# Kernel optimization log

Measured on AMD Instinct MI355X. Metric: run time of the kernel, lower is better.

Reference implementation:

```python
import jax, jax.numpy as jnp
import numpy as np

B, N, IN_CH = 4, 8192, 4
K = 16
W0, W1, W2 = 64, 128, 256
NUM_CLASSES = 3


def setup_inputs() -> dict:
    key = jax.random.key(0)
    ks = jax.random.split(key, 16)

    def lin(kw, kb, fan_in, fan_out):
        bound = 1.0 / np.sqrt(fan_in)
        w = jax.random.uniform(kw, (fan_in, fan_out), jnp.float32, -bound, bound)
        b = jax.random.uniform(kb, (fan_out,), jnp.float32, -bound, bound)
        return w, b

    x = jax.random.normal(ks[0], (B, N, IN_CH), jnp.float32)
    stem_w, stem_b = lin(ks[1], ks[2], IN_CH, W0)
    b1_w, b1_b = lin(ks[3], ks[4], 2 * W0 + 3, W1)
    b2_w, b2_b = lin(ks[5], ks[6], 2 * W1 + 3, W2)
    glob_w, glob_b = lin(ks[7], ks[8], W2, W2)
    head1_w, head1_b = lin(ks[9], ks[10], 2 * W2, W2)
    head2_w, head2_b = lin(ks[11], ks[12], W2, NUM_CLASSES)
    return {
        'x': x,
        'hmix_a': jnp.float32(1.0), 'hmix_b': jnp.float32(1.0), 'hmix_c': jnp.float32(0.0),
        'stem_w': stem_w, 'stem_b': stem_b,
        'b1_w': b1_w, 'b1_b': b1_b,
        'b2_w': b2_w, 'b2_b': b2_b,
        'glob_w': glob_w, 'glob_b': glob_b,
        'head1_w': head1_w, 'head1_b': head1_b,
        'head2_w': head2_w, 'head2_b': head2_b,
        'thresh': jnp.float32(0.15), 'sharp': jnp.float32(10.0), 'scale': jnp.float32(0.5),
    }


def _knn_idx(coords, k):
    # coords: [B,N,3] -> idx of k nearest neighbors (incl. self), no grad.
    c = jax.lax.stop_gradient(coords)
    xx = jnp.sum(c * c, axis=-1, keepdims=True)            # [B,N,1]
    dist = xx + jnp.swapaxes(xx, 1, 2) - 2.0 * jnp.einsum('bnc,bmc->bnm', c, c)
    dist = jnp.maximum(dist, 0.0)
    _, idx = jax.lax.top_k(-dist, k)                       # smallest distances
    return idx                                             # [B,N,k]


def _local_agg(coords, feat, idx, w, b):
    # gather-concat-MLP-maxpool, faithful to LocalAggBlock (pool='max')
    bidx = jnp.arange(coords.shape[0])[:, None, None]
    nb_f = feat[bidx, idx]                                 # [B,N,k,C]
    nb_p = coords[bidx, idx]                               # [B,N,k,3]
    fi = feat[:, :, None, :]
    pi = coords[:, :, None, :]
    h = jnp.concatenate(
        [jnp.broadcast_to(fi, nb_f.shape), nb_f - fi, nb_p - pi], axis=-1)
    h = jax.nn.relu(jnp.einsum('bnkd,do->bnko', h, w) + b)
    return jnp.max(h, axis=2)                              # [B,N,out]


def reference(x, hmix_a, hmix_b, hmix_c, stem_w, stem_b, b1_w, b1_b,
              b2_w, b2_b, glob_w, glob_b, head1_w, head1_b,
              head2_w, head2_b, thresh, sharp, scale):
    # HeightMixer: z_eff = a*z + b*hag + c
    z_eff = hmix_a * x[..., 2] + hmix_b * x[..., 3] + hmix_c
    coords = jnp.stack([x[..., 0], x[..., 1], z_eff], axis=-1)  # [B,N,3]

    f = jax.nn.relu(x @ stem_w + stem_b)                   # stem: [B,N,64]

    # both blocks use the same coords -> same KNN graph; compute once
    idx = _knn_idx(coords, K)
    f = _local_agg(coords, f, idx, b1_w, b1_b)             # [B,N,128]
    f = _local_agg(coords, f, idx, b2_w, b2_b)             # [B,N,256]

    g = jnp.max(f, axis=1)                                 # [B,256]
    g = jax.nn.relu(g @ glob_w + glob_b)
    g = jnp.broadcast_to(g[:, None, :], f.shape)           # [B,N,256]

    h = jnp.concatenate([f, g], axis=-1)                   # [B,N,512]
    h = jax.nn.relu(h @ head1_w + head1_b)
    logits = h @ head2_w + head2_b                         # [B,N,3]

    # HeightPriorBias on class 0
    hag = x[..., 3]
    bias = scale * jax.nn.sigmoid(sharp * (thresh - hag))
    logits = logits.at[..., 0].add(bias)
    return logits
```

## Files before the change

kernel.cpp:

```cpp
#include <hip/hip_runtime.h>
#include <math.h>

typedef unsigned long long u64;
typedef unsigned int u32;
typedef _Float16 h8v __attribute__((ext_vector_type(8)));
typedef float    f4v __attribute__((ext_vector_type(4)));
typedef float    f16v __attribute__((ext_vector_type(16)));
typedef float    f2v __attribute__((ext_vector_type(2)));

#define MFMA16(a,b,c) __builtin_amdgcn_mfma_f32_16x16x32_f16(a, b, c, 0, 0, 0)
#define MFMA32(a,b,c) __builtin_amdgcn_mfma_f32_32x32x16_f16(a, b, c, 0, 0, 0)

#define B_ 4
#define N_ 8192
#define K_ 16
#define W0_ 64
#define W1_ 128
#define W2_ 256
#define X0_ 96
#define X1_ 160
#define QAD_ 16
#define CAP_ 128

__global__ __launch_bounds__(256) void prep_kernel(
    const float* __restrict__ x,
    const float* __restrict__ stem_w, const float* __restrict__ stem_b,
    const float* __restrict__ hmix_a, const float* __restrict__ hmix_b,
    const float* __restrict__ hmix_c,
    float* __restrict__ coords4, _Float16* __restrict__ fx0,
    _Float16* __restrict__ fx1,
    const float* __restrict__ b1_w, const float* __restrict__ b2_w,
    const float* __restrict__ h1w,
    _Float16* __restrict__ w1m, _Float16* __restrict__ w1d,
    _Float16* __restrict__ w2m, _Float16* __restrict__ w2d,
    _Float16* __restrict__ h1wT,
    _Float16* __restrict__ qa, _Float16* __restrict__ cbq,
    float* __restrict__ part) {
  const int bi = blockIdx.x;
  const int tid = threadIdx.x;
  const int PB = (B_*N_)/4;
  if (bi < PB) {
    const int p = bi * 4 + (tid >> 6);
    const int o = tid & 63;
    const float x0 = x[p*4+0], x1 = x[p*4+1], x2 = x[p*4+2], x3 = x[p*4+3];
    const float z = hmix_a[0]*x2 + hmix_b[0]*x3 + hmix_c[0];
    float acc = stem_b[o] + x0*stem_w[0*W0_+o] + x1*stem_w[1*W0_+o]
              + x2*stem_w[2*W0_+o] + x3*stem_w[3*W0_+o];
    fx0[p*X0_+o] = (_Float16)fmaxf(acc, 0.f);
    if (o < 32) {
      const float tv = (o==0) ? x0 : (o==1) ? x1 : (o==2) ? z : 0.f;
      fx0[p*X0_+W0_+o] = (_Float16)tv;
      fx1[(size_t)p*X1_+W1_+o] = (_Float16)tv;
    }
    if (o == 0) {
      const float xx = x0*x0 + x1*x1 + z*z;
      ((float4*)coords4)[p] = make_float4(x0, x1, z, xx);
    } else if (o == 1) {
      const _Float16 hx = (_Float16)x0, hy = (_Float16)x1, hz = (_Float16)z;
      const _Float16 lx = (_Float16)(x0 - (float)hx);
      const _Float16 ly = (_Float16)(x1 - (float)hy);
      const _Float16 lz = (_Float16)(z  - (float)hz);
      const _Float16 one = (_Float16)1.f, Z = (_Float16)0.f;
      h8v a0 = {hx, hy, hz, lx, ly, lz, hx, hy};
      h8v a1 = {hz, lx, ly, lz, one, one, Z, Z};
      *(h8v*)(qa + (size_t)p*QAD_)      = a0;
      *(h8v*)(qa + (size_t)p*QAD_ + 8)  = a1;
    } else if (o == 2) {
      const _Float16 hx = (_Float16)x0, hy = (_Float16)x1, hz = (_Float16)z;
      const _Float16 lx = (_Float16)(x0 - (float)hx);
      const _Float16 ly = (_Float16)(x1 - (float)hy);
      const _Float16 lz = (_Float16)(z  - (float)hz);
      const float xx = x0*x0 + x1*x1 + z*z;
      const _Float16 xh = (_Float16)xx;
      const _Float16 xl = (_Float16)(xx - (float)xh);
      const _Float16 nhx = (_Float16)(-2.f*(float)hx);
      const _Float16 nhy = (_Float16)(-2.f*(float)hy);
      const _Float16 nhz = (_Float16)(-2.f*(float)hz);
      const _Float16 nlx = (_Float16)(-2.f*(float)lx);
      const _Float16 nly = (_Float16)(-2.f*(float)ly);
      const _Float16 nlz = (_Float16)(-2.f*(float)lz);
      const _Float16 Z = (_Float16)0.f;
      h8v b0 = {nhx, nhy, nhz, nlx, nly, nlz, nlx, nly};
      h8v b1 = {nlz, nhx, nhy, nhz, xh, xl, Z, Z};
      *(h8v*)(cbq + (size_t)p*QAD_)      = b0;
      *(h8v*)(cbq + (size_t)p*QAD_ + 8)  = b1;
    }
  } else if (bi < PB + W1_) {
    const int o = bi - PB, c = tid;
    if (c < X0_) {
      float mv = 0.f, dv = 0.f;
      if (c < W0_)        { const float wm = b1_w[(W0_+c)*W1_+o]; mv = wm; dv = b1_w[c*W1_+o] - wm; }
      else if (c < W0_+3) { const float wp = b1_w[(2*W0_+(c-W0_))*W1_+o]; mv = wp; dv = -wp; }
      w1m[o*X0_+c] = (_Float16)mv;
      w1d[o*X0_+c] = (_Float16)dv;
    }
  } else if (bi < PB + W1_ + W2_) {
    const int o = bi - PB - W1_, c = tid;
    if (c < X1_) {
      float mv = 0.f, dv = 0.f;
      if (c < W1_)        { const float wm = b2_w[(W1_+c)*W2_+o]; mv = wm; dv = b2_w[c*W2_+o] - wm; }
      else if (c < W1_+3) { const float wp = b2_w[(2*W1_+(c-W1_))*W2_+o]; mv = wp; dv = -wp; }
      w2m[o*X1_+c] = (_Float16)mv;
      w2d[o*X1_+c] = (_Float16)dv;
    }
  } else if (bi < PB + W1_ + 2*W2_) {
    const int o = bi - PB - W1_ - W2_;
    for (int c = tid; c < 512; c += 256)
      h1wT[(size_t)o*512 + c] = (_Float16)h1w[(size_t)c*256 + o];
  } else {
    ((float4*)part)[tid] = make_float4(0.f, 0.f, 0.f, 0.f);
  }
}

#define DPP_MIN(v, ctrl)                                                        \
  { const int _t = __builtin_amdgcn_update_dpp(0, __float_as_int(v),            \
      ctrl, 0xF, 0xF, false);                                                   \
    v = fminf(v, __int_as_float(_t)); }

__device__ __forceinline__ float sixteenth_of_minima(float v) {
  float th = 0.f;
#pragma unroll
  for (int r = 0; r < 16; ++r) {
    float w = v;
    DPP_MIN(w, 0x111); DPP_MIN(w, 0x112); DPP_MIN(w, 0x114); DPP_MIN(w, 0x118);
    DPP_MIN(w, 0x142); DPP_MIN(w, 0x143);
    const float mv = __int_as_float(
        __builtin_amdgcn_readlane(__float_as_int(w), 63));
    th = mv;
    v = (v == mv) ? INFINITY : v;
  }
  return th;
}

#define KNN_DIST2(dA, dB)                                                       \
  const f2v cjx = {cj.x, cj.x}, cjy = {cj.y, cj.y},                             \
            cjz = {cj.z, cj.z}, cjw = {cj.w, cj.w};                             \
  f2v tA = cAx * cjx;                                                           \
  tA = __builtin_elementwise_fma(cAy, cjy, tA);                                 \
  tA = __builtin_elementwise_fma(cAz, cjz, tA);                                 \
  const f2v dA = __builtin_elementwise_fma(tA, m2, cAw + cjw);                  \
  f2v tB = cBx * cjx;                                                           \
  tB = __builtin_elementwise_fma(cBy, cjy, tB);                                 \
  tB = __builtin_elementwise_fma(cBz, cjz, tB);                                 \
  const f2v dB = __builtin_elementwise_fma(tB, m2, cBw + cjw);

__global__ __launch_bounds__(512) void knn_kernel(
    const float* __restrict__ coords4, const _Float16* __restrict__ qa,
    const _Float16* __restrict__ cbq, int* __restrict__ knn_idx) {
  const int tid = threadIdx.x;
  const int wid = tid >> 6;
  const int lane = tid & 63;
  const int p0 = blockIdx.x * 32;
  const int bb = (p0 >> 13) << 13;

  __shared__ float  s_Tp[32];
  __shared__ float  s_Tpr[32];
  __shared__ int    s_cnt[32];
  __shared__ float2 s_pr[32][CAP_];
  if (tid < 32) s_cnt[tid] = 0;

  const float4* cb = ((const float4*)coords4) + bb;
  const int q0 = p0 + wid * 4;
  const float4 c0 = ((const float4*)coords4)[q0+0];
  const float4 c1 = ((const float4*)coords4)[q0+1];
  const float4 c2 = ((const float4*)coords4)[q0+2];
  const float4 c3 = ((const float4*)coords4)[q0+3];
  const f2v m2 = {-2.f, -2.f};
  const f2v cAx = {c0.x, c1.x}, cAy = {c0.y, c1.y}, cAz = {c0.z, c1.z}, cAw = {c0.w, c1.w};
  const f2v cBx = {c2.x, c3.x}, cBy = {c2.y, c3.y}, cBz = {c2.z, c3.z}, cBw = {c2.w, c3.w};

  float lm0 = INFINITY, lm1 = INFINITY, lm2 = INFINITY, lm3 = INFINITY;
  for (int it = 0; it < 64; ++it) {
    const float4 cj = cb[it*64 + lane];
    KNN_DIST2(dA, dB)
    lm0 = fminf(lm0, fmaxf(dA[0], 0.f));
    lm1 = fminf(lm1, fmaxf(dA[1], 0.f));
    lm2 = fminf(lm2, fmaxf(dB[0], 0.f));
    lm3 = fminf(lm3, fmaxf(dB[1], 0.f));
  }
  const float Th0 = sixteenth_of_minima(lm0);
  const float Th1 = sixteenth_of_minima(lm1);
  const float Th2 = sixteenth_of_minima(lm2);
  const float Th3 = sixteenth_of_minima(lm3);
  if (lane == 0) {
    s_Tp[wid*4+0] = Th0 - c0.w + (1e-3f + 1e-5f*c0.w);
    s_Tp[wid*4+1] = Th1 - c1.w + (1e-3f + 1e-5f*c1.w);
    s_Tp[wid*4+2] = Th2 - c2.w + (1e-3f + 1e-5f*c2.w);
    s_Tp[wid*4+3] = Th3 - c3.w + (1e-3f + 1e-5f*c3.w);
  }
  __syncthreads();
  if (tid < 32) {
    const int h = tid >> 4, r = tid & 15;
    s_Tpr[tid] = s_Tp[(r&3) + 8*(r>>2) + 4*h];
  }
  __syncthreads();

  const int half = lane >> 5;
  const int h4 = half << 2;
  const int lrow = lane & 31;
  float Tv[16];
  *(f4v*)&Tv[0]  = *(const f4v*)&s_Tpr[half*16 + 0];
  *(f4v*)&Tv[4]  = *(const f4v*)&s_Tpr[half*16 + 4];
  *(f4v*)&Tv[8]  = *(const f4v*)&s_Tpr[half*16 + 8];
  *(f4v*)&Tv[12] = *(const f4v*)&s_Tpr[half*16 + 12];
  const h8v afrag = *(const h8v*)(qa + (size_t)(p0 + lrow)*QAD_ + half*8);
  const int c0b = wid * 1024;
  const int cibase = c0b + lrow;
  const _Float16* cbp = cbq + (size_t)(bb + c0b + lrow)*QAD_ + half*8;
  const f16v zacc = (f16v)0.0f;

  h8v bcur = *(const h8v*)cbp;
#pragma unroll 2
  for (int t = 0; t < 32; ++t) {
    const h8v bnxt = *(const h8v*)(cbp + (size_t)((t < 31) ? (t+1) : 0) * 32 * QAD_);
    const f16v acc = MFMA32(afrag, bcur, zacc);
#pragma unroll
    for (int r = 0; r < 16; ++r) {
      const bool c = acc[r] < Tv[r];
      const u64 m = __ballot(c);
      if (m) {
        const int q = ((r&3) + 8*(r>>2)) + h4;
        if (c) {
          const int pos = atomicAdd(&s_cnt[q], 1);
          if (pos < CAP_)
            s_pr[q][pos] = make_float2(acc[r], __int_as_float(cibase + t*32));
        }
      }
    }
    bcur = bnxt;
  }
  __syncthreads();

  for (int qq = 0; qq < 4; ++qq) {
    const int q = wid*4 + qq;
    const int cnt = s_cnt[q];
    const int L = (cnt < CAP_) ? cnt : CAP_;
    float d0 = INFINITY, d1 = INFINITY;
    int   i0 = 0x7fffffff, i1 = 0x7fffffff;
    if (lane < L)      { const float2 e = s_pr[q][lane];      d0 = e.x; i0 = __float_as_int(e.y); }
    if (lane + 64 < L) { const float2 e = s_pr[q][lane + 64]; d1 = e.x; i1 = __float_as_int(e.y); }
    int keep = 0;
    for (int r = 0; r < K_; ++r) {
      float dl = d0; int il = i0; bool s1 = false;
      if (d1 < dl || (d1 == dl && i1 < il)) { dl = d1; il = i1; s1 = true; }
      float w = dl;
      DPP_MIN(w, 0x111); DPP_MIN(w, 0x112); DPP_MIN(w, 0x114); DPP_MIN(w, 0x118);
      DPP_MIN(w, 0x142); DPP_MIN(w, 0x143);
      const float dmin = __int_as_float(
          __builtin_amdgcn_readlane(__float_as_int(w), 63));
      u64 m = __ballot(dl == dmin);
      int bi = 0x7fffffff, bl = 0;
      do {
        const int s = (int)__ffsll((unsigned long long)m) - 1; m &= m - 1;
        const int ii = __builtin_amdgcn_readlane(il, s);
        if (ii < bi) { bi = ii; bl = s; }
      } while (m);
      if (lane == bl) { if (s1) d1 = INFINITY; else d0 = INFINITY; }
      if (lane == r) keep = bi;
    }
    if (lane < K_) knn_idx[(size_t)(p0 + q)*K_ + lane] = keep;
  }
}

template<int KS, int NPASS, bool GMAX>
__global__ __launch_bounds__(256) void aggm_kernel(
    const _Float16* __restrict__ fx, const int* __restrict__ knn_idx,
    const _Float16* __restrict__ midT, const _Float16* __restrict__ difT,
    const float* __restrict__ bw,
    _Float16* __restrict__ fo, const int ostr, u32* __restrict__ part) {
  const int XD  = KS*32;
  const int XDP = XD + 8;
  const int CH  = KS*4;
  const int p0 = blockIdx.x * 16;
  const int bb = (p0 >> 13) << 13;
  const int tid = threadIdx.x;
  const int w = tid >> 6, lane = tid & 63, col = lane & 15, quad = lane >> 4;
  const int koff = quad * 8;

  __shared__ int s_idx[256];
  __shared__ _Float16 sA[2][64*(KS*32+8)];

  s_idx[tid] = knn_idx[p0*K_ + tid];

  f4v cacc[NPASS][2];
  {
    h8v Ao[KS];
    const _Float16* ap = fx + (size_t)(p0+col)*XD + koff;
#pragma unroll
    for (int kk = 0; kk < KS; ++kk) Ao[kk] = *(const h8v*)(ap + kk*32);
#pragma unroll
    for (int ps = 0; ps < NPASS; ++ps) {
      const int o0 = ps*128 + w*32;
      const _Float16* b0 = difT + (size_t)(o0 + col)*XD + koff;
      const _Float16* b1 = difT + (size_t)(o0 + 16 + col)*XD + koff;
      f4v c0 = {0.f,0.f,0.f,0.f}, c1 = {0.f,0.f,0.f,0.f};
#pragma unroll
      for (int kk = 0; kk < KS; ++kk) {
        c0 = MFMA16(Ao[kk], *(const h8v*)(b0 + kk*32), c0);
        c1 = MFMA16(Ao[kk], *(const h8v*)(b1 + kk*32), c1);
      }
      cacc[ps][0] = c0; cacc[ps][1] = c1;
    }
  }

  h8v Bf[NPASS][2][KS];
  float bias[NPASS][2];
#pragma unroll
  for (int ps = 0; ps < NPASS; ++ps) {
    const int o0 = ps*128 + w*32;
#pragma unroll
    for (int kk = 0; kk < KS; ++kk) {
      Bf[ps][0][kk] = *(const h8v*)(midT + (size_t)(o0 + col)*XD + kk*32 + koff);
      Bf[ps][1][kk] = *(const h8v*)(midT + (size_t)(o0 + 16 + col)*XD + kk*32 + koff);
    }
    bias[ps][0] = bw[o0 + col];
    bias[ps][1] = bw[o0 + 16 + col];
  }
  __syncthreads();

  for (int c = tid; c < 64*CH; c += 256) {
    const int r = c / CH, o = c - r*CH;
    *(uint4*)&sA[0][r*XDP + o*8] =
        *(const uint4*)(fx + (size_t)(bb + s_idx[((r&15)<<4) + (r>>4)])*XD + o*8);
  }
  __syncthreads();

  f4v M[NPASS][2];
#pragma unroll
  for (int ps = 0; ps < NPASS; ++ps) {
    M[ps][0] = (f4v){-INFINITY,-INFINITY,-INFINITY,-INFINITY};
    M[ps][1] = (f4v){-INFINITY,-INFINITY,-INFINITY,-INFINITY};
  }

  for (int s = 0; s < 4; ++s) {
    const int buf = s & 1;
    if (s < 3) {
      for (int c = tid; c < 64*CH; c += 256) {
        const int r = c / CH, o = c - r*CH;
        *(uint4*)&sA[buf^1][r*XDP + o*8] =
            *(const uint4*)(fx + (size_t)(bb + s_idx[((r&15)<<4) + 4*s+4 + (r>>4)])*XD + o*8);
      }
    }
#pragma unroll
    for (int half = 0; half < 4; ++half) {
      h8v Ac[KS];
      const _Float16* ap = &sA[buf][(half*16 + col)*XDP + koff];
#pragma unroll
      for (int kk = 0; kk < KS; ++kk) Ac[kk] = *(const h8v*)(ap + kk*32);
#pragma unroll
      for (int ps = 0; ps < NPASS; ++ps) {
        f4v d0 = {0.f,0.f,0.f,0.f}, d1 = {0.f,0.f,0.f,0.f};
#pragma unroll
        for (int kk = 0; kk < KS; ++kk) {
          d0 = MFMA16(Ac[kk], Bf[ps][0][kk], d0);
          d1 = MFMA16(Ac[kk], Bf[ps][1][kk], d1);
        }
#pragma unroll
        for (int e = 0; e < 4; ++e) {
          M[ps][0][e] = fmaxf(M[ps][0][e], d0[e]);
          M[ps][1][e] = fmaxf(M[ps][1][e], d1[e]);
        }
      }
    }
    if (s < 3) __syncthreads();
  }

  const int prow = p0 + (quad << 2);
  const int bq = p0 >> 13;
#pragma unroll
  for (int ps = 0; ps < NPASS; ++ps) {
    const int o0 = ps*128 + w*32;
    const int oa = o0 + col, ob = oa + 16;
    float v0[4], v1[4];
#pragma unroll
    for (int reg = 0; reg < 4; ++reg) {
      v0[reg] = fmaxf(M[ps][0][reg] + cacc[ps][0][reg] + bias[ps][0], 0.f);
      v1[reg] = fmaxf(M[ps][1][reg] + cacc[ps][1][reg] + bias[ps][1], 0.f);
      fo[(size_t)(prow+reg)*ostr + oa] = (_Float16)v0[reg];
      fo[(size_t)(prow+reg)*ostr + ob] = (_Float16)v1[reg];
    }
    if (GMAX) {
      float bm0 = fmaxf(fmaxf(v0[0], v0[1]), fmaxf(v0[2], v0[3]));
      float bm1 = fmaxf(fmaxf(v1[0], v1[1]), fmaxf(v1[2], v1[3]));
      bm0 = fmaxf(bm0, __shfl_xor(bm0, 16, 64));
      bm0 = fmaxf(bm0, __shfl_xor(bm0, 32, 64));
      bm1 = fmaxf(bm1, __shfl_xor(bm1, 16, 64));
      bm1 = fmaxf(bm1, __shfl_xor(bm1, 32, 64));
      if (quad == 0) {
        atomicMax(part + bq*W2_ + oa, __float_as_uint(bm0));
        atomicMax(part + bq*W2_ + ob, __float_as_uint(bm1));
      }
    }
  }
}

__global__ __launch_bounds__(256) void gfc_kernel(
    const float* __restrict__ part, const float* __restrict__ gw,
    const float* __restrict__ gb, _Float16* __restrict__ g2h) {
  const int b = blockIdx.x;
  const int o = threadIdx.x;
  __shared__ float s_g[W2_];
  s_g[o] = part[b*W2_ + o];
  __syncthreads();
  float acc = gb[o];
  for (int d = 0; d < W2_; ++d) acc += s_g[d]*gw[d*W2_ + o];
  g2h[b*W2_ + o] = (_Float16)fmaxf(acc, 0.f);
}

__global__ __launch_bounds__(256) void headm_kernel(
    const _Float16* __restrict__ f2h, const _Float16* __restrict__ g2h,
    const _Float16* __restrict__ h1wT, const float* __restrict__ h1b,
    const float* __restrict__ h2w, const float* __restrict__ h2b,
    const float* __restrict__ x,
    const float* __restrict__ thresh, const float* __restrict__ sharp,
    const float* __restrict__ scale,
    float* __restrict__ out) {
  const int p0 = blockIdx.x * 32;
  const int b = p0 >> 13;
  const int tid = threadIdx.x;
  const int w = tid >> 6, lane = tid & 63, col = lane & 15, quad = lane >> 4;

  __shared__ _Float16 sA[32*520];
  __shared__ float    sh[32*260];

  for (int t = tid; t < 32*32; t += 256) {
    const int r = t >> 5, cc = (t & 31) * 8;
    *(uint4*)&sA[r*520 + cc] = *(const uint4*)&f2h[(size_t)(p0+r)*W2_ + cc];
  }
  for (int t = tid; t < 32*32; t += 256) {
    const int r = t >> 5, cc = (t & 31) * 8;
    *(uint4*)&sA[r*520 + 256 + cc] = *(const uint4*)&g2h[b*W2_ + cc];
  }
  __syncthreads();

  f4v acc[2][4];
#pragma unroll
  for (int r = 0; r < 2; ++r)
#pragma unroll
    for (int t = 0; t < 4; ++t) acc[r][t] = (f4v){0.f,0.f,0.f,0.f};

  for (int kk = 0; kk < 16; ++kk) {
    const h8v a0 = *(const h8v*)&sA[col*520 + kk*32 + quad*8];
    const h8v a1 = *(const h8v*)&sA[(16+col)*520 + kk*32 + quad*8];
#pragma unroll
    for (int t = 0; t < 4; ++t) {
      const h8v bt = *(const h8v*)&h1wT[(size_t)(w*64 + t*16 + col)*512 + kk*32 + quad*8];
      acc[0][t] = MFMA16(a0, bt, acc[0][t]);
      acc[1][t] = MFMA16(a1, bt, acc[1][t]);
    }
  }
#pragma unroll
  for (int r = 0; r < 2; ++r)
#pragma unroll
    for (int t = 0; t < 4; ++t) {
      const int o = w*64 + t*16 + col;
      const float bv = h1b[o];
#pragma unroll
      for (int reg = 0; reg < 4; ++reg)
        sh[(r*16 + quad*4 + reg)*260 + o] = fmaxf(acc[r][t][reg] + bv, 0.f);
    }
  __syncthreads();

  if (tid < 96) {
    const int pp = tid / 3, c = tid % 3;
    float s = h2b[c];
    for (int d = 0; d < 256; ++d) s += sh[pp*260 + d] * h2w[d*3 + c];
    if (c == 0) {
      const float hag = x[(size_t)(p0+pp)*4 + 3];
      s += scale[0] / (1.f + expf(-sharp[0]*(thresh[0] - hag)));
    }
    out[(size_t)(p0+pp)*3 + c] = s;
  }
}

extern "C" void kernel_launch(void* const* d_in, const int* in_sizes, int n_in,
                              void* d_out, int out_size, void* d_ws, size_t ws_size,
                              hipStream_t stream) {
  const float* x       = (const float*)d_in[0];
  const float* hmix_a  = (const float*)d_in[1];
  const float* hmix_b  = (const float*)d_in[2];
  const float* hmix_c  = (const float*)d_in[3];
  const float* stem_w  = (const float*)d_in[4];
  const float* stem_b  = (const float*)d_in[5];
  const float* b1_w    = (const float*)d_in[6];
  const float* b1_b    = (const float*)d_in[7];
  const float* b2_w    = (const float*)d_in[8];
  const float* b2_b    = (const float*)d_in[9];
  const float* glob_w  = (const float*)d_in[10];
  const float* glob_b  = (const float*)d_in[11];
  const float* head1_w = (const float*)d_in[12];
  const float* head1_b = (const float*)d_in[13];
  const float* head2_w = (const float*)d_in[14];
  const float* head2_b = (const float*)d_in[15];
  const float* thresh  = (const float*)d_in[16];
  const float* sharp   = (const float*)d_in[17];
  const float* scale   = (const float*)d_in[18];
  float* out = (float*)d_out;

  char* base = (char*)d_ws;
  float*     coords4 = (float*)    (base + 0);
  int*       idxb    = (int*)      (base + 524288);
  _Float16*  fx0     = (_Float16*) (base + 2621440);
  _Float16*  fx1     = (_Float16*) (base + 8912896);
  _Float16*  f2h     = (_Float16*) (base + 19398656);
  _Float16*  qa      = (_Float16*) (base + 19398656);
  _Float16*  cbq     = (_Float16*) (base + 20447232);
  _Float16*  w1m     = (_Float16*) (base + 36175872);
  _Float16*  w1d     = (_Float16*) (base + 36200448);
  _Float16*  w2m     = (_Float16*) (base + 36225024);
  _Float16*  w2d     = (_Float16*) (base + 36306944);
  _Float16*  h1wT    = (_Float16*) (base + 36388864);
  float*     part    = (float*)    (base + 36651008);
  _Float16*  g2h     = (_Float16*) (base + 36782080);
  const int NP = B_ * N_;

  prep_kernel<<<NP/4 + W1_ + 2*W2_ + 1, 256, 0, stream>>>(
      x, stem_w, stem_b, hmix_a, hmix_b, hmix_c, coords4, fx0, fx1,
      b1_w, b2_w, head1_w, w1m, w1d, w2m, w2d, h1wT, qa, cbq, part);
  knn_kernel<<<NP/32, 512, 0, stream>>>(coords4, qa, cbq, idxb);
  aggm_kernel<3, 1, false><<<NP/16, 256, 0, stream>>>(
      fx0, idxb, w1m, w1d, b1_b, fx1, X1_, (u32*)0);
  aggm_kernel<5, 2, true><<<NP/16, 256, 0, stream>>>(
      fx1, idxb, w2m, w2d, b2_b, f2h, W2_, (u32*)part);
  gfc_kernel<<<B_, 256, 0, stream>>>(part, glob_w, glob_b, g2h);
  headm_kernel<<<NP/32, 256, 0, stream>>>(f2h, g2h, h1wT, head1_b, head2_w, head2_b,
                                          x, thresh, sharp, scale, out);
}
```

Before: 375.8 us.

## Compute KNN threshold pass with MFMA distances instead of scalar fp32 loop

The first KNN pass, which finds a per-query threshold from the minimum distance of each candidate slice, now uses the same fp16 MFMA distance products as the candidate collection pass instead of a scalar fp32 FMA loop over coords4. Per-lane minima are reduced through a shared buffer that aliases the candidate pool. The threshold is now exact in the MFMA metric, so the comparison becomes <= and no epsilon slack is needed. A single-register fast path handles the selection when at most 64 candidates are found. This replaces the costly fp32 scalar distance loop with tensor-core work, but relies on fp16 rounding for the threshold, which can change neighbor selection near ties.

```diff
diff --git a/kernel.cpp b/kernel.cpp
--- a/kernel.cpp
+++ b/kernel.cpp
@@ -132,61 +132,64 @@
   return th;
 }
 
-#define KNN_DIST2(dA, dB)                                                       \
-  const f2v cjx = {cj.x, cj.x}, cjy = {cj.y, cj.y},                             \
-            cjz = {cj.z, cj.z}, cjw = {cj.w, cj.w};                             \
-  f2v tA = cAx * cjx;                                                           \
-  tA = __builtin_elementwise_fma(cAy, cjy, tA);                                 \
-  tA = __builtin_elementwise_fma(cAz, cjz, tA);                                 \
-  const f2v dA = __builtin_elementwise_fma(tA, m2, cAw + cjw);                  \
-  f2v tB = cBx * cjx;                                                           \
-  tB = __builtin_elementwise_fma(cBy, cjy, tB);                                 \
-  tB = __builtin_elementwise_fma(cBz, cjz, tB);                                 \
-  const f2v dB = __builtin_elementwise_fma(tB, m2, cBw + cjw);
-
 __global__ __launch_bounds__(512) void knn_kernel(
-    const float* __restrict__ coords4, const _Float16* __restrict__ qa,
-    const _Float16* __restrict__ cbq, int* __restrict__ knn_idx) {
+    const _Float16* __restrict__ qa, const _Float16* __restrict__ cbq,
+    int* __restrict__ knn_idx) {
   const int tid = threadIdx.x;
   const int wid = tid >> 6;
   const int lane = tid & 63;
   const int p0 = blockIdx.x * 32;
   const int bb = (p0 >> 13) << 13;
 
-  __shared__ float  s_Tp[32];
-  __shared__ float  s_Tpr[32];
-  __shared__ int    s_cnt[32];
-  __shared__ float2 s_pr[32][CAP_];
+  __shared__ float s_pool[32*CAP_*2];
+  __shared__ float s_Tp[32];
+  __shared__ float s_Tpr[32];
+  __shared__ int   s_cnt[32];
+  float2* const s_pr  = (float2*)s_pool;
+  float*  const t_min = s_pool;
   if (tid < 32) s_cnt[tid] = 0;
 
-  const float4* cb = ((const float4*)coords4) + bb;
-  const int q0 = p0 + wid * 4;
-  const float4 c0 = ((const float4*)coords4)[q0+0];
-  const float4 c1 = ((const float4*)coords4)[q0+1];
-  const float4 c2 = ((const float4*)coords4)[q0+2];
-  const float4 c3 = ((const float4*)coords4)[q0+3];
-  const f2v m2 = {-2.f, -2.f};
-  const f2v cAx = {c0.x, c1.x}, cAy = {c0.y, c1.y}, cAz = {c0.z, c1.z}, cAw = {c0.w, c1.w};
-  const f2v cBx = {c2.x, c3.x}, cBy = {c2.y, c3.y}, cBz = {c2.z, c3.z}, cBw = {c2.w, c3.w};
-
-  float lm0 = INFINITY, lm1 = INFINITY, lm2 = INFINITY, lm3 = INFINITY;
-  for (int it = 0; it < 64; ++it) {
-    const float4 cj = cb[it*64 + lane];
-    KNN_DIST2(dA, dB)
-    lm0 = fminf(lm0, fmaxf(dA[0], 0.f));
-    lm1 = fminf(lm1, fmaxf(dA[1], 0.f));
-    lm2 = fminf(lm2, fmaxf(dB[0], 0.f));
-    lm3 = fminf(lm3, fmaxf(dB[1], 0.f));
-  }
-  const float Th0 = sixteenth_of_minima(lm0);
-  const float Th1 = sixteenth_of_minima(lm1);
-  const float Th2 = sixteenth_of_minima(lm2);
-  const float Th3 = sixteenth_of_minima(lm3);
-  if (lane == 0) {
-    s_Tp[wid*4+0] = Th0 - c0.w + (1e-3f + 1e-5f*c0.w);
-    s_Tp[wid*4+1] = Th1 - c1.w + (1e-3f + 1e-5f*c1.w);
-    s_Tp[wid*4+2] = Th2 - c2.w + (1e-3f + 1e-5f*c2.w);
-    s_Tp[wid*4+3] = Th3 - c3.w + (1e-3f + 1e-5f*c3.w);
+  const int half = lane >> 5;
+  const int h4 = half << 2;
+  const int lrow = lane & 31;
+  const h8v afrag = *(const h8v*)(qa + (size_t)(p0 + lrow)*QAD_ + half*8);
+  const int c0b = wid * 1024;
+  const int cibase = c0b + lrow;
+  const _Float16* cbp = cbq + (size_t)(bb + c0b + lrow)*QAD_ + half*8;
+  const f16v zacc = (f16v)0.0f;
+
+  float gmin[16];
+  h8v bcur = *(const h8v*)cbp;
+  {
+    const h8v b1 = *(const h8v*)(cbp + 32*QAD_);
+    const f16v a0 = MFMA32(afrag, bcur, zacc);
+#pragma unroll
+    for (int r = 0; r < 16; ++r) gmin[r] = a0[r];
+    bcur = b1;
+  }
+#pragma unroll 2
+  for (int t = 1; t < 32; ++t) {
+    const h8v bnxt = *(const h8v*)(cbp + (size_t)((t < 31) ? (t+1) : 0) * 32 * QAD_);
+    const f16v acc = MFMA32(afrag, bcur, zacc);
+#pragma unroll
+    for (int r = 0; r < 16; ++r) gmin[r] = fminf(gmin[r], acc[r]);
+    bcur = bnxt;
+  }
+
+  {
+    float* tb = t_min + (h4*256 + wid*32 + lrow);
+#pragma unroll
+    for (int r = 0; r < 16; ++r)
+      tb[((r&3) + 8*(r>>2))*256] = gmin[r];
+  }
+  __syncthreads();
+
+  for (int qq = 0; qq < 4; ++qq) {
+    const int q = wid*4 + qq;
+    const f4v gv = *(const f4v*)&t_min[q*256 + lane*4];
+    const float lm = fminf(fminf(gv[0], gv[1]), fminf(gv[2], gv[3]));
+    const float T = sixteenth_of_minima(lm);
+    if (lane == 0) s_Tp[q] = T;
   }
   __syncthreads();
   if (tid < 32) {
@@ -195,35 +198,25 @@
   }
   __syncthreads();
 
-  const int half = lane >> 5;
-  const int h4 = half << 2;
-  const int lrow = lane & 31;
   float Tv[16];
   *(f4v*)&Tv[0]  = *(const f4v*)&s_Tpr[half*16 + 0];
   *(f4v*)&Tv[4]  = *(const f4v*)&s_Tpr[half*16 + 4];
   *(f4v*)&Tv[8]  = *(const f4v*)&s_Tpr[half*16 + 8];
   *(f4v*)&Tv[12] = *(const f4v*)&s_Tpr[half*16 + 12];
-  const h8v afrag = *(const h8v*)(qa + (size_t)(p0 + lrow)*QAD_ + half*8);
-  const int c0b = wid * 1024;
-  const int cibase = c0b + lrow;
-  const _Float16* cbp = cbq + (size_t)(bb + c0b + lrow)*QAD_ + half*8;
-  const f16v zacc = (f16v)0.0f;
-
-  h8v bcur = *(const h8v*)cbp;
 #pragma unroll 2
   for (int t = 0; t < 32; ++t) {
     const h8v bnxt = *(const h8v*)(cbp + (size_t)((t < 31) ? (t+1) : 0) * 32 * QAD_);
     const f16v acc = MFMA32(afrag, bcur, zacc);
 #pragma unroll
     for (int r = 0; r < 16; ++r) {
-      const bool c = acc[r] < Tv[r];
+      const bool c = acc[r] <= Tv[r];
       const u64 m = __ballot(c);
       if (m) {
         const int q = ((r&3) + 8*(r>>2)) + h4;
         if (c) {
           const int pos = atomicAdd(&s_cnt[q], 1);
           if (pos < CAP_)
-            s_pr[q][pos] = make_float2(acc[r], __int_as_float(cibase + t*32));
+            s_pr[q*CAP_ + pos] = make_float2(acc[r], __int_as_float(cibase + t*32));
         }
       }
     }
@@ -235,28 +228,49 @@
     const int q = wid*4 + qq;
     const int cnt = s_cnt[q];
     const int L = (cnt < CAP_) ? cnt : CAP_;
-    float d0 = INFINITY, d1 = INFINITY;
-    int   i0 = 0x7fffffff, i1 = 0x7fffffff;
-    if (lane < L)      { const float2 e = s_pr[q][lane];      d0 = e.x; i0 = __float_as_int(e.y); }
-    if (lane + 64 < L) { const float2 e = s_pr[q][lane + 64]; d1 = e.x; i1 = __float_as_int(e.y); }
     int keep = 0;
-    for (int r = 0; r < K_; ++r) {
-      float dl = d0; int il = i0; bool s1 = false;
-      if (d1 < dl || (d1 == dl && i1 < il)) { dl = d1; il = i1; s1 = true; }
-      float w = dl;
-      DPP_MIN(w, 0x111); DPP_MIN(w, 0x112); DPP_MIN(w, 0x114); DPP_MIN(w, 0x118);
-      DPP_MIN(w, 0x142); DPP_MIN(w, 0x143);
-      const float dmin = __int_as_float(
-          __builtin_amdgcn_readlane(__float_as_int(w), 63));
-      u64 m = __ballot(dl == dmin);
-      int bi = 0x7fffffff, bl = 0;
-      do {
-        const int s = (int)__ffsll((unsigned long long)m) - 1; m &= m - 1;
-        const int ii = __builtin_amdgcn_readlane(il, s);
-        if (ii < bi) { bi = ii; bl = s; }
-      } while (m);
-      if (lane == bl) { if (s1) d1 = INFINITY; else d0 = INFINITY; }
-      if (lane == r) keep = bi;
+    if (L <= 64) {
+      float d0 = INFINITY; int i0 = 0x7fffffff;
+      if (lane < L) { const float2 e = s_pr[q*CAP_ + lane]; d0 = e.x; i0 = __float_as_int(e.y); }
+      for (int r = 0; r < K_; ++r) {
+        float w = d0;
+        DPP_MIN(w, 0x111); DPP_MIN(w, 0x112); DPP_MIN(w, 0x114); DPP_MIN(w, 0x118);
+        DPP_MIN(w, 0x142); DPP_MIN(w, 0x143);
+        const float dmin = __int_as_float(
+            __builtin_amdgcn_readlane(__float_as_int(w), 63));
+        u64 m = __ballot(d0 == dmin);
+        int bi = 0x7fffffff, bl = 0;
+        do {
+          const int s = (int)__ffsll((unsigned long long)m) - 1; m &= m - 1;
+          const int ii = __builtin_amdgcn_readlane(i0, s);
+          if (ii < bi) { bi = ii; bl = s; }
+        } while (m);
+        if (lane == bl) d0 = INFINITY;
+        if (lane == r) keep = bi;
+      }
+    } else {
+      float d0 = INFINITY, d1 = INFINITY;
+      int   i0 = 0x7fffffff, i1 = 0x7fffffff;
+      if (lane < L)      { const float2 e = s_pr[q*CAP_ + lane];      d0 = e.x; i0 = __float_as_int(e.y); }
+      if (lane + 64 < L) { const float2 e = s_pr[q*CAP_ + lane + 64]; d1 = e.x; i1 = __float_as_int(e.y); }
+      for (int r = 0; r < K_; ++r) {
+        float dl = d0; int il = i0; bool s1 = false;
+        if (d1 < dl || (d1 == dl && i1 < il)) { dl = d1; il = i1; s1 = true; }
+        float w = dl;
+        DPP_MIN(w, 0x111); DPP_MIN(w, 0x112); DPP_MIN(w, 0x114); DPP_MIN(w, 0x118);
+        DPP_MIN(w, 0x142); DPP_MIN(w, 0x143);
+        const float dmin = __int_as_float(
+            __builtin_amdgcn_readlane(__float_as_int(w), 63));
+        u64 m = __ballot(dl == dmin);
+        int bi = 0x7fffffff, bl = 0;
+        do {
+          const int s = (int)__ffsll((unsigned long long)m) - 1; m &= m - 1;
+          const int ii = __builtin_amdgcn_readlane(il, s);
+          if (ii < bi) { bi = ii; bl = s; }
+        } while (m);
+        if (lane == bl) { if (s1) d1 = INFINITY; else d0 = INFINITY; }
+        if (lane == r) keep = bi;
+      }
     }
     if (lane < K_) knn_idx[(size_t)(p0 + q)*K_ + lane] = keep;
   }
@@ -517,7 +531,7 @@
   prep_kernel<<<NP/4 + W1_ + 2*W2_ + 1, 256, 0, stream>>>(
       x, stem_w, stem_b, hmix_a, hmix_b, hmix_c, coords4, fx0, fx1,
       b1_w, b2_w, head1_w, w1m, w1d, w2m, w2d, h1wT, qa, cbq, part);
-  knn_kernel<<<NP/32, 512, 0, stream>>>(coords4, qa, cbq, idxb);
+  knn_kernel<<<NP/32, 512, 0, stream>>>(qa, cbq, idxb);
   aggm_kernel<3, 1, false><<<NP/16, 256, 0, stream>>>(
       fx0, idxb, w1m, w1d, b1_b, fx1, X1_, (u32*)0);
   aggm_kernel<5, 2, true><<<NP/16, 256, 0, stream>>>(
```

After: 378.0 us. No clear change (+0.6%).
